# Performance work log

Hardware: AMD Instinct MI355X
Metric: run time of the kernel (lower is better)

Reference implementation:

```python
import jax, jax.numpy as jnp
import numpy as np

N_HEAD = 16
EPS = 1e-5
ROPE_BASE = 10000.0


def setup_inputs() -> dict:
    key = jax.random.key(0)
    ks = jax.random.split(key, 6)
    B, T, C = 2, 2048, 1024
    s = 0.02  # typical GPT init scale
    return {
        "x": jax.random.normal(ks[0], (B, T, C), dtype=jnp.float32),
        "wq": jax.random.normal(ks[1], (C, C), dtype=jnp.float32) * s,
        "wk": jax.random.normal(ks[2], (C, C), dtype=jnp.float32) * s,
        "wv": jax.random.normal(ks[3], (C, C), dtype=jnp.float32) * s,
        "wproj": jax.random.normal(ks[4], (C, C), dtype=jnp.float32) * s,
        "g_rms": jnp.ones((C // N_HEAD,), dtype=jnp.float32),
    }


def reference(x, wq, wk, wv, wproj, g_rms):
    B, T, C = x.shape
    H = N_HEAD
    hd = C // H

    # QKV projections (torch Linear: y = x @ W.T), split into heads -> [B,T,H,hd]
    q = (x @ wq.T).reshape(B, T, H, hd)
    k = (x @ wk.T).reshape(B, T, H, hd)
    v = (x @ wv.T).reshape(B, T, H, hd)

    # RMSNorm over head_dim on q and k
    def rms(t):
        var = jnp.mean(t * t, axis=-1, keepdims=True) + EPS
        return g_rms * (t * jax.lax.rsqrt(var))

    q, k = rms(q), rms(k)

    # Rotary embeddings: cos/sin cached in bf16 in the original -> bf16 round-trip
    inv_freq = 1.0 / (ROPE_BASE ** (jnp.arange(0, hd, 2, dtype=jnp.float32) / hd))
    freqs = jnp.outer(jnp.arange(T, dtype=jnp.float32), inv_freq)  # [T, hd/2]
    cos = jnp.cos(freqs).astype(jnp.bfloat16).astype(jnp.float32)[None, :, None, :]
    sin = jnp.sin(freqs).astype(jnp.bfloat16).astype(jnp.float32)[None, :, None, :]

    def rope(u):
        d = hd // 2
        u1, u2 = u[..., :d], u[..., d:]
        return jnp.concatenate([u1 * cos + u2 * sin, -u1 * sin + u2 * cos], axis=-1)

    q, k = rope(q), rope(k)

    # Attention: float ones attn_mask => constant +1.0 bias (softmax-invariant);
    # NOT causal (is_causal defaults False); dropout_p = 0.
    qh = q.transpose(0, 2, 1, 3)  # [B,H,T,hd]
    kh = k.transpose(0, 2, 1, 3)
    vh = v.transpose(0, 2, 1, 3)
    scale = 1.0 / jnp.sqrt(jnp.float32(hd))
    scores = jnp.einsum('bhtd,bhsd->bhts', qh, kh) * scale + 1.0  # [B,H,T,T]
    attn = jax.nn.softmax(scores, axis=-1)
    y = jnp.einsum('bhts,bhsd->bhtd', attn, vh)

    y = y.transpose(0, 2, 1, 3).reshape(B, T, C)
    return y @ wproj.T
```

## Files before the change

### kernel.cpp

```cpp
#include <hip/hip_runtime.h>
#include <hip/hip_bf16.h>
#include <stdint.h>

typedef __attribute__((ext_vector_type(8))) short short8;
typedef __attribute__((ext_vector_type(4))) float f32x4;
typedef __attribute__((ext_vector_type(16))) float f32x16;
typedef __attribute__((ext_vector_type(4))) unsigned short ushort4v;
typedef __attribute__((ext_vector_type(4))) unsigned int uint4v;

#define TT 2048
#define HH 16
#define CCdim 1024
#define BT 4096
#define LOG2E 1.44269504088896f

__device__ inline unsigned short f2bf(float f) {
  unsigned u = __float_as_uint(f);
  u += 0x7FFF + ((u >> 16) & 1);
  return (unsigned short)(u >> 16);
}
__device__ inline float bf2f(unsigned short s) {
  return __uint_as_float(((unsigned)s) << 16);
}
__device__ inline unsigned pack2(float a, float b) {
  return (unsigned)f2bf(a) | ((unsigned)f2bf(b) << 16);
}
__device__ inline unsigned cvtpk(float lo, float hi) {
  unsigned r;
  asm("v_cvt_pk_bf16_f32 %0, %1, %2" : "=v"(r) : "v"(lo), "v"(hi));
  return r;
}
__device__ inline void plswap(unsigned &a, unsigned &b) {
  asm("v_permlane32_swap_b32 %0, %1" : "+v"(a), "+v"(b));
}

__device__ inline void gload16(const unsigned short* g, unsigned short* l) {
  __builtin_amdgcn_global_load_lds((const __attribute__((address_space(1))) void*)g,
                                   (__attribute__((address_space(3))) void*)l, 16, 0, 0);
}

#define VMB(N) do { asm volatile("s_waitcnt vmcnt(" #N ")" ::: "memory"); \
                    __builtin_amdgcn_s_barrier(); \
                    __builtin_amdgcn_sched_barrier(0); } while (0)

__global__ __launch_bounds__(256) void prep(const float* __restrict__ x, const float* __restrict__ wq,
                     const float* __restrict__ wk, const float* __restrict__ wv,
                     const float* __restrict__ wp, unsigned short* __restrict__ xb,
                     unsigned short* __restrict__ wqkv, unsigned short* __restrict__ wpb,
                     float2* __restrict__ tab) {
  long idx = ((long)blockIdx.x * 256 + threadIdx.x) * 4;
  const long NX = (long)BT * CCdim;
  const long NW = (long)CCdim * CCdim;
  auto cvt4 = [](const float* src, unsigned short* dst, long off) {
    float4 v = *(const float4*)(src + off);
    ushort4v o = { f2bf(v.x), f2bf(v.y), f2bf(v.z), f2bf(v.w) };
    *(ushort4v*)(dst + off) = o;
  };
  if (idx < NX) { cvt4(x, xb, idx); return; }
  idx -= NX;
  if (idx < NW) { cvt4(wq, wqkv, idx); return; }
  idx -= NW;
  if (idx < NW) { cvt4(wk, wqkv + NW, idx); return; }
  idx -= NW;
  if (idx < NW) { cvt4(wv, wqkv + 2 * NW, idx); return; }
  idx -= NW;
  if (idx < NW) { cvt4(wp, wpb, idx); return; }
  idx -= NW;
  if (idx < (long)TT * 32) {
#pragma unroll
    for (int j = 0; j < 4; ++j) {
      long e = idx + j;
      int t = (int)(e >> 5), i = (int)(e & 31);
      float invf = powf(10000.0f, -(float)i / 32.0f);
      float a = (float)t * invf;
      tab[e] = make_float2(bf2f(f2bf(cosf(a))), bf2f(f2bf(sinf(a))));
    }
  }
}

__global__ __launch_bounds__(256) void gemm_qkv(const unsigned short* __restrict__ A,
                                                const unsigned short* __restrict__ W,
                                                const float* __restrict__ g,
                                                const float2* __restrict__ tab,
                                                unsigned short* __restrict__ Qh,
                                                unsigned short* __restrict__ Kp,
                                                unsigned short* __restrict__ Vp) {
  __shared__ __align__(16) char smem[49152];
  unsigned short* const S0 = (unsigned short*)smem;
  unsigned short* const S1 = S0 + 8192;
  unsigned short* const S2 = S0 + 16384;
  typedef unsigned short (*Earr)[64][68];
  Earr E = (Earr)smem;
  const int K = 1024;
  const int tid = threadIdx.x;
  const int lane = tid & 63;
  const int wid = tid >> 6;
  const int wr = wid >> 1, wc = wid & 1;
  const int m0 = blockIdx.y * 128;
  const int n0 = blockIdx.x * 128;

  f32x4 acc[4][4] = {};

  const int srow0 = tid >> 2;
  const int cgrp = tid & 3;
  const int cd = (cgrp ^ ((srow0 >> 1) & 3)) * 8;
  const unsigned short* Arow0 = A + (long)(m0 + srow0) * K + cd;
  const unsigned short* Arow1 = A + (long)(m0 + srow0 + 64) * K + cd;
  const unsigned short* Wrow0 = W + (long)(n0 + srow0) * K + cd;
  const unsigned short* Wrow1 = W + (long)(n0 + srow0 + 64) * K + cd;

  auto stage = [&](unsigned short* Ab, int kt) {
    const int kof = kt * 32;
    gload16(Arow0 + kof, Ab + wid * 512);
    gload16(Arow1 + kof, Ab + 2048 + wid * 512);
    gload16(Wrow0 + kof, Ab + 4096 + wid * 512);
    gload16(Wrow1 + kof, Ab + 6144 + wid * 512);
  };
  auto compute = [&](const unsigned short* Ab) {
    const unsigned short* Wb = Ab + 4096;
    short8 af[4], bf[4];
#pragma unroll
    for (int mi = 0; mi < 4; ++mi) {
      int r = wr * 64 + mi * 16 + (lane & 15);
      af[mi] = *(const short8*)&Ab[r * 32 + (((lane >> 4) ^ ((r >> 1) & 3)) * 8)];
    }
#pragma unroll
    for (int nj = 0; nj < 4; ++nj) {
      int r = wc * 64 + nj * 16 + (lane & 15);
      bf[nj] = *(const short8*)&Wb[r * 32 + (((lane >> 4) ^ ((r >> 1) & 3)) * 8)];
    }
#pragma unroll
    for (int mi = 0; mi < 4; ++mi)
#pragma unroll
      for (int nj = 0; nj < 4; ++nj)
        acc[mi][nj] = __builtin_amdgcn_mfma_f32_16x16x32_bf16(af[mi], bf[nj], acc[mi][nj], 0, 0, 0);
  };

  stage(S0, 0);
  stage(S1, 1);
  for (int tb = 0; tb < 30; tb += 3) {
    VMB(4); stage(S2, tb + 2); compute(S0);
    VMB(4); stage(S0, tb + 3); compute(S1);
    VMB(4); stage(S1, tb + 4); compute(S2);
  }
  VMB(4); compute(S0);
  VMB(0); compute(S1);
  __syncthreads();

  const int type = blockIdx.x >> 3;
  const int c0 = n0 + wc * 64;
  const int b = m0 >> 11;
  const int t0w = (m0 & 2047) + wr * 64;
  const int bh = b * 16 + ((c0 >> 6) & 15);
  const int cl = lane & 15;
  const int hi4 = lane >> 4;

  if (type < 2) {
    float gv0 = g[cl], gv1 = g[cl + 16], gv2 = g[cl + 32], gv3 = g[cl + 48];
    const float qs = (type == 0) ? 0.125f * LOG2E : 1.0f;
#pragma unroll
    for (int mi = 0; mi < 4; ++mi)
#pragma unroll
      for (int j = 0; j < 4; ++j) {
        float x0 = acc[mi][0][j], x1 = acc[mi][1][j], x2 = acc[mi][2][j], x3 = acc[mi][3][j];
        float ss = x0 * x0 + x1 * x1 + x2 * x2 + x3 * x3;
        ss += __shfl_xor(ss, 1); ss += __shfl_xor(ss, 2);
        ss += __shfl_xor(ss, 4); ss += __shfl_xor(ss, 8);
        float ri = rsqrtf(ss * (1.0f / 64.0f) + 1e-5f);
        float xn0 = x0 * ri * gv0, xn1 = x1 * ri * gv1;
        float xn2 = x2 * ri * gv2, xn3 = x3 * ri * gv3;
        int t = t0w + mi * 16 + 4 * hi4 + j;
        float2 cs0 = tab[t * 32 + cl];
        float2 cs1 = tab[t * 32 + cl + 16];
        int lr = mi * 16 + 4 * hi4 + j;
        E[wid][lr][cl]      = f2bf((xn0 * cs0.x + xn2 * cs0.y) * qs);
        E[wid][lr][cl + 16] = f2bf((xn1 * cs1.x + xn3 * cs1.y) * qs);
        E[wid][lr][cl + 32] = f2bf((xn2 * cs0.x - xn0 * cs0.y) * qs);
        E[wid][lr][cl + 48] = f2bf((xn3 * cs1.x - xn1 * cs1.y) * qs);
      }
  } else {
#pragma unroll
    for (int mi = 0; mi < 4; ++mi)
#pragma unroll
      for (int j = 0; j < 4; ++j) {
        int lr = mi * 16 + 4 * hi4 + j;
        E[wid][lr][cl]      = f2bf(acc[mi][0][j]);
        E[wid][lr][cl + 16] = f2bf(acc[mi][1][j]);
        E[wid][lr][cl + 32] = f2bf(acc[mi][2][j]);
        E[wid][lr][cl + 48] = f2bf(acc[mi][3][j]);
      }
  }
  __syncthreads();

  if (type == 0) {
    for (int row = 0; row < 64; ++row) {
      int t = t0w + row;
      Qh[((long)bh * TT + t) * 64 + lane] = E[wid][row][lane];
    }
  } else if (type == 1) {
    for (int row = 0; row < 64; ++row) {
      int t = t0w + row;
      Kp[(((long)bh * 64 + (t >> 5)) * 4 + (lane >> 4)) * 512
         + ((t & 31) + 32 * ((lane >> 3) & 1)) * 8 + (lane & 7)] = E[wid][row][lane];
    }
  } else {
    unsigned short* base = Vp + ((long)bh * 64 + (t0w >> 5)) * 2048;
#pragma unroll
    for (int it = 0; it < 8; ++it) {
      int id = it * 64 + lane;
      int cc = it & 1, sd = (it >> 1) & 1, ttloc = (it >> 2) & 1;
      int d = sd * 32 + (lane & 31);
      int tl = ttloc * 32 + cc * 16 + (lane >> 5) * 8;
      short8 o;
#pragma unroll
      for (int jj = 0; jj < 8; ++jj) o[jj] = (short)E[wid][tl + jj][d];
      *(short8*)(base + (long)id * 8) = o;
    }
  }
}

__global__ __launch_bounds__(256) void gemm_bt(const unsigned short* __restrict__ A,
                                               const unsigned short* __restrict__ W,
                                               float* __restrict__ C, int ldc) {
  __shared__ __align__(16) unsigned short Sbuf[3][8192];
  unsigned short* const S0 = &Sbuf[0][0];
  unsigned short* const S1 = &Sbuf[1][0];
  unsigned short* const S2 = &Sbuf[2][0];
  const int K = 1024;
  const int tid = threadIdx.x;
  const int lane = tid & 63;
  const int wid = tid >> 6;
  const int wr = wid >> 1, wc = wid & 1;
  const int m0 = blockIdx.y * 128;
  const int n0 = blockIdx.x * 128;

  f32x4 acc[4][4] = {};

  const int srow0 = tid >> 2;
  const int cgrp = tid & 3;
  const int cd = (cgrp ^ ((srow0 >> 1) & 3)) * 8;
  const unsigned short* Arow0 = A + (long)(m0 + srow0) * K + cd;
  const unsigned short* Arow1 = A + (long)(m0 + srow0 + 64) * K + cd;
  const unsigned short* Wrow0 = W + (long)(n0 + srow0) * K + cd;
  const unsigned short* Wrow1 = W + (long)(n0 + srow0 + 64) * K + cd;

  auto stage = [&](unsigned short* Ab, int kt) {
    const int kof = kt * 32;
    gload16(Arow0 + kof, Ab + wid * 512);
    gload16(Arow1 + kof, Ab + 2048 + wid * 512);
    gload16(Wrow0 + kof, Ab + 4096 + wid * 512);
    gload16(Wrow1 + kof, Ab + 6144 + wid * 512);
  };
  auto compute = [&](const unsigned short* Ab) {
    const unsigned short* Wb = Ab + 4096;
    short8 af[4], bf[4];
#pragma unroll
    for (int mi = 0; mi < 4; ++mi) {
      int r = wr * 64 + mi * 16 + (lane & 15);
      af[mi] = *(const short8*)&Ab[r * 32 + (((lane >> 4) ^ ((r >> 1) & 3)) * 8)];
    }
#pragma unroll
    for (int nj = 0; nj < 4; ++nj) {
      int r = wc * 64 + nj * 16 + (lane & 15);
      bf[nj] = *(const short8*)&Wb[r * 32 + (((lane >> 4) ^ ((r >> 1) & 3)) * 8)];
    }
#pragma unroll
    for (int mi = 0; mi < 4; ++mi)
#pragma unroll
      for (int nj = 0; nj < 4; ++nj)
        acc[mi][nj] = __builtin_amdgcn_mfma_f32_16x16x32_bf16(af[mi], bf[nj], acc[mi][nj], 0, 0, 0);
  };

  stage(S0, 0);
  stage(S1, 1);
  for (int tb = 0; tb < 30; tb += 3) {
    VMB(4); stage(S2, tb + 2); compute(S0);
    VMB(4); stage(S0, tb + 3); compute(S1);
    VMB(4); stage(S1, tb + 4); compute(S2);
  }
  VMB(4); compute(S0);
  VMB(0); compute(S1);

#pragma unroll
  for (int mi = 0; mi < 4; ++mi)
#pragma unroll
    for (int nj = 0; nj < 4; ++nj)
#pragma unroll
      for (int j = 0; j < 4; ++j) {
        int rr = m0 + wr * 64 + mi * 16 + 4 * (lane >> 4) + j;
        int ncol = n0 + wc * 64 + nj * 16 + (lane & 15);
        C[(long)rr * ldc + ncol] = acc[mi][nj][j];
      }
}

__global__ __launch_bounds__(256, 2) void attn(const unsigned short* __restrict__ Qh,
                                               const unsigned short* __restrict__ Kp,
                                               const unsigned short* __restrict__ Vp,
                                               float* __restrict__ Opart,
                                               float* __restrict__ L) {
  const int lane = threadIdx.x & 63;
  const int wid = threadIdx.x >> 6;
  int bid = blockIdx.x;
  bid = (bid & 7) * 64 + (bid >> 3);
  const int w = bid * 4 + wid;
  const int qt = w & 31;
  const int half = (w >> 5) & 1;
  const int bh = w >> 6;
  const long bhT = (long)bh * TT;
  const int q0 = qt * 64;
  const int l31 = lane & 31;
  const int hk = (lane >> 5) * 8;

  short8 qf[4], qg[4];
  {
    const unsigned short* qp = Qh + (bhT + q0 + l31) * 64 + hk;
#pragma unroll
    for (int c = 0; c < 4; ++c) {
      qf[c] = *(const short8*)(qp + c * 16);
      qg[c] = *(const short8*)(qp + 2048 + c * 16);
    }
  }

  const unsigned short* kp = Kp + ((long)(bh * 64 + half * 32)) * 2048 + lane * 8;
  const unsigned short* vp = Vp + ((long)(bh * 64 + half * 32)) * 2048 + lane * 8;

  f32x16 oacc0 = {}, oacc1 = {}, oacc2 = {}, oacc3 = {};
  float ell = 0.f, ell2 = 0.f;

  short8 kA[4], vA0[2], vA1[2], kB[4], vB0[2], vB1[2];
#pragma unroll
  for (int c = 0; c < 4; ++c) kA[c] = *(const short8*)(kp + c * 512);
#pragma unroll
  for (int c = 0; c < 2; ++c) {
    vA0[c] = *(const short8*)(vp + c * 512);
    vA1[c] = *(const short8*)(vp + 1024 + c * 512);
  }

  auto body = [&](short8 (&kc)[4], short8 (&v0c)[2], short8 (&v1c)[2],
                  short8 (&knx)[4], short8 (&v0n)[2], short8 (&v1n)[2], int tn) {
    const unsigned short* kpn = kp + tn * 2048;
    const unsigned short* vpn = vp + tn * 2048;
#pragma unroll
    for (int c = 0; c < 4; ++c) knx[c] = *(const short8*)(kpn + c * 512);
#pragma unroll
    for (int c = 0; c < 2; ++c) {
      v0n[c] = *(const short8*)(vpn + c * 512);
      v1n[c] = *(const short8*)(vpn + 1024 + c * 512);
    }

    __builtin_amdgcn_s_setprio(1);
    f32x16 s = {}, s2 = {};
#pragma unroll
    for (int c = 0; c < 4; ++c) {
      s  = __builtin_amdgcn_mfma_f32_32x32x16_bf16(kc[c], qf[c], s, 0, 0, 0);
      s2 = __builtin_amdgcn_mfma_f32_32x32x16_bf16(kc[c], qg[c], s2, 0, 0, 0);
    }
    __builtin_amdgcn_s_setprio(0);

#pragma unroll
    for (int r = 0; r < 16; ++r) s[r] = __builtin_amdgcn_exp2f(s[r]);
#pragma unroll
    for (int r = 0; r < 16; ++r) s2[r] = __builtin_amdgcn_exp2f(s2[r]);
    {
      float t0 = s[0] + s[1], t1 = s[2] + s[3], t2s = s[4] + s[5], t3 = s[6] + s[7];
      float t4 = s[8] + s[9], t5 = s[10] + s[11], t6 = s[12] + s[13], t7 = s[14] + s[15];
      t0 += t1; t2s += t3; t4 += t5; t6 += t7;
      ell += (t0 + t2s) + (t4 + t6);
    }
    {
      float t0 = s2[0] + s2[1], t1 = s2[2] + s2[3], t2s = s2[4] + s2[5], t3 = s2[6] + s2[7];
      float t4 = s2[8] + s2[9], t5 = s2[10] + s2[11], t6 = s2[12] + s2[13], t7 = s2[14] + s2[15];
      t0 += t1; t2s += t3; t4 += t5; t6 += t7;
      ell2 += (t0 + t2s) + (t4 + t6);
    }

    unsigned a0 = cvtpk(s[0], s[1]),   a1 = cvtpk(s[2], s[3]);
    unsigned a2 = cvtpk(s[4], s[5]),   a3 = cvtpk(s[6], s[7]);
    unsigned a4 = cvtpk(s[8], s[9]),   a5 = cvtpk(s[10], s[11]);
    unsigned a6 = cvtpk(s[12], s[13]), a7 = cvtpk(s[14], s[15]);
    plswap(a0, a2); plswap(a1, a3); plswap(a4, a6); plswap(a5, a7);
    uint4v f0 = { a0, a1, a2, a3 };
    uint4v f1 = { a4, a5, a6, a7 };
    short8 pf0 = __builtin_bit_cast(short8, f0);
    short8 pf1 = __builtin_bit_cast(short8, f1);

    unsigned b0 = cvtpk(s2[0], s2[1]),   b1 = cvtpk(s2[2], s2[3]);
    unsigned b2 = cvtpk(s2[4], s2[5]),   b3 = cvtpk(s2[6], s2[7]);
    unsigned b4 = cvtpk(s2[8], s2[9]),   b5 = cvtpk(s2[10], s2[11]);
    unsigned b6 = cvtpk(s2[12], s2[13]), b7 = cvtpk(s2[14], s2[15]);
    plswap(b0, b2); plswap(b1, b3); plswap(b4, b6); plswap(b5, b7);
    uint4v g0 = { b0, b1, b2, b3 };
    uint4v g1 = { b4, b5, b6, b7 };
    short8 pg0 = __builtin_bit_cast(short8, g0);
    short8 pg1 = __builtin_bit_cast(short8, g1);

    __builtin_amdgcn_s_setprio(1);
    oacc0 = __builtin_amdgcn_mfma_f32_32x32x16_bf16(v0c[0], pf0, oacc0, 0, 0, 0);
    oacc0 = __builtin_amdgcn_mfma_f32_32x32x16_bf16(v0c[1], pf1, oacc0, 0, 0, 0);
    oacc1 = __builtin_amdgcn_mfma_f32_32x32x16_bf16(v1c[0], pf0, oacc1, 0, 0, 0);
    oacc1 = __builtin_amdgcn_mfma_f32_32x32x16_bf16(v1c[1], pf1, oacc1, 0, 0, 0);
    oacc2 = __builtin_amdgcn_mfma_f32_32x32x16_bf16(v0c[0], pg0, oacc2, 0, 0, 0);
    oacc2 = __builtin_amdgcn_mfma_f32_32x32x16_bf16(v0c[1], pg1, oacc2, 0, 0, 0);
    oacc3 = __builtin_amdgcn_mfma_f32_32x32x16_bf16(v1c[0], pg0, oacc3, 0, 0, 0);
    oacc3 = __builtin_amdgcn_mfma_f32_32x32x16_bf16(v1c[1], pg1, oacc3, 0, 0, 0);
    __builtin_amdgcn_s_setprio(0);
  };

  for (int t = 0; t < 32; t += 2) {
    int t1 = t + 1;
    int t2 = (t < 30) ? (t + 2) : 31;
    body(kA, vA0, vA1, kB, vB0, vB1, t1);
    body(kB, vB0, vB1, kA, vA0, vA1, t2);
  }

  float ellf  = ell + __shfl_xor(ell, 32);
  float ellf2 = ell2 + __shfl_xor(ell2, 32);
  const long prow = (long)(half * 32 + bh) * TT + q0 + l31;
  float* orow  = Opart + prow * 64;
  float* orow2 = orow + 32 * 64;
  const int dhalf = 4 * (lane >> 5);
#pragma unroll
  for (int i = 0; i < 8; ++i) {
    int d = (2 * i & 3) + 8 * (i >> 1) + dhalf;
    *(float2*)&orow[d]       = make_float2(oacc0[2 * i], oacc0[2 * i + 1]);
    *(float2*)&orow[32 + d]  = make_float2(oacc1[2 * i], oacc1[2 * i + 1]);
    *(float2*)&orow2[d]      = make_float2(oacc2[2 * i], oacc2[2 * i + 1]);
    *(float2*)&orow2[32 + d] = make_float2(oacc3[2 * i], oacc3[2 * i + 1]);
  }
  if (lane < 32) { L[prow] = ellf; L[prow + 32] = ellf2; }
}

__global__ __launch_bounds__(256) void combine(const float* __restrict__ Opart,
                                               const float* __restrict__ L,
                                               unsigned short* __restrict__ Y) {
  const long HALF = (long)32 * TT * 64;
  int idx = blockIdx.x * 256 + threadIdx.x;
  int row = idx >> 5;
  int d = (idx & 31) * 2;
  float2 o0 = *(const float2*)&Opart[(long)row * 64 + d];
  float2 o1 = *(const float2*)&Opart[HALF + (long)row * 64 + d];
  float rinv = 1.0f / (L[row] + L[65536 + row]);
  float ox = (o0.x + o1.x) * rinv;
  float oy = (o0.y + o1.y) * rinv;
  int bh = row >> 11, qrow = row & (TT - 1);
  int b = bh >> 4, h = bh & 15;
  *(unsigned*)&Y[((long)(b * TT + qrow)) * CCdim + h * 64 + d] = pack2(ox, oy);
}

extern "C" void kernel_launch(void* const* d_in, const int* in_sizes, int n_in,
                              void* d_out, int out_size, void* d_ws, size_t ws_size,
                              hipStream_t stream) {
  const float* x  = (const float*)d_in[0];
  const float* wq = (const float*)d_in[1];
  const float* wk = (const float*)d_in[2];
  const float* wv = (const float*)d_in[3];
  const float* wp = (const float*)d_in[4];
  const float* g  = (const float*)d_in[5];

  char* w = (char*)d_ws;
  unsigned short* xb   = (unsigned short*)w; w += (long)BT * CCdim * 2;
  unsigned short* wqkv = (unsigned short*)w; w += (long)3 * CCdim * CCdim * 2;
  unsigned short* wpb  = (unsigned short*)w; w += (long)CCdim * CCdim * 2;
  unsigned short* qh   = (unsigned short*)w; w += (long)BT * CCdim * 2;
  unsigned short* kp   = (unsigned short*)w; w += (long)BT * CCdim * 2;
  unsigned short* vp   = (unsigned short*)w; w += (long)BT * CCdim * 2;
  unsigned short* yb   = (unsigned short*)w; w += (long)BT * CCdim * 2;
  float2* tab          = (float2*)w;         w += (long)TT * 32 * 8;
  float* Opart         = (float*)w;          w += (long)64 * TT * 64 * 4;
  float* Lbuf          = (float*)w;          w += (long)64 * TT * 4;

  long total = ((long)BT * CCdim + 4L * CCdim * CCdim + (long)TT * 32) / 4;
  int pblocks = (int)((total + 255) / 256);
  prep<<<pblocks, 256, 0, stream>>>(x, wq, wk, wv, wp, xb, wqkv, wpb, tab);
  gemm_qkv<<<dim3(24, 32), 256, 0, stream>>>(xb, wqkv, g, tab, qh, kp, vp);
  attn<<<512, 256, 0, stream>>>(qh, kp, vp, Opart, Lbuf);
  combine<<<8192, 256, 0, stream>>>(Opart, Lbuf, yb);
  gemm_bt<<<dim3(8, 32), 256, 0, stream>>>(yb, wpb, (float*)d_out, 1024);
}
```

Before: 127.4 us.

## Fuse split-KV combine into attention via LDS and swizzle GEMM blocks per XCD

The attention kernel now puts both KV halves of a query tile in the same workgroup. One wave writes its partial output and row sums to LDS, and the partner wave merges them, normalizes, and writes bf16 Y directly. This removes the fp32 partial-output round trip through global memory and the separate combine launch. Both GEMMs also remap block indices so each XCD works on a contiguous group of tiles, which should improve L2 reuse. The cost is extra LDS use in attention (about 33KB) and a block-wide barrier, which may reduce occupancy.

```diff
diff --git a/kernel.cpp b/kernel.cpp
--- a/kernel.cpp
+++ b/kernel.cpp
@@ -96,8 +96,12 @@
   const int lane = tid & 63;
   const int wid = tid >> 6;
   const int wr = wid >> 1, wc = wid & 1;
-  const int m0 = blockIdx.y * 128;
-  const int n0 = blockIdx.x * 128;
+  const int bid0 = blockIdx.y * 24 + blockIdx.x;
+  const int xcd = bid0 & 7, ii = bid0 >> 3;
+  const int bx = (xcd & 1) * 12 + ii % 12;
+  const int by = (xcd >> 1) * 8 + ii / 12;
+  const int m0 = by * 128;
+  const int n0 = bx * 128;
 
   f32x4 acc[4][4] = {};
 
@@ -147,7 +151,7 @@
   VMB(0); compute(S1);
   __syncthreads();
 
-  const int type = blockIdx.x >> 3;
+  const int type = bx >> 3;
   const int c0 = n0 + wc * 64;
   const int b = m0 >> 11;
   const int t0w = (m0 & 2047) + wr * 64;
@@ -231,8 +235,10 @@
   const int lane = tid & 63;
   const int wid = tid >> 6;
   const int wr = wid >> 1, wc = wid & 1;
-  const int m0 = blockIdx.y * 128;
-  const int n0 = blockIdx.x * 128;
+  const int bid0 = blockIdx.y * 8 + blockIdx.x;
+  const int xcd = bid0 & 7, ii = bid0 >> 3;
+  const int m0 = (xcd * 4 + ii / 8) * 128;
+  const int n0 = (ii & 7) * 128;
 
   f32x4 acc[4][4] = {};
 
@@ -296,15 +302,16 @@
 __global__ __launch_bounds__(256, 2) void attn(const unsigned short* __restrict__ Qh,
                                                const unsigned short* __restrict__ Kp,
                                                const unsigned short* __restrict__ Vp,
-                                               float* __restrict__ Opart,
-                                               float* __restrict__ L) {
+                                               unsigned short* __restrict__ Y) {
+  __shared__ __align__(16) float Obuf[2][64][65];
+  __shared__ float Ebuf[2][64];
   const int lane = threadIdx.x & 63;
   const int wid = threadIdx.x >> 6;
   int bid = blockIdx.x;
   bid = (bid & 7) * 64 + (bid >> 3);
   const int w = bid * 4 + wid;
-  const int qt = w & 31;
-  const int half = (w >> 5) & 1;
+  const int half = w & 1;
+  const int qt = (w >> 1) & 31;
   const int bh = w >> 6;
   const long bhT = (long)bh * TT;
   const int q0 = qt * 64;
@@ -415,36 +422,44 @@
 
   float ellf  = ell + __shfl_xor(ell, 32);
   float ellf2 = ell2 + __shfl_xor(ell2, 32);
-  const long prow = (long)(half * 32 + bh) * TT + q0 + l31;
-  float* orow  = Opart + prow * 64;
-  float* orow2 = orow + 32 * 64;
+  const int pl = wid >> 1;
   const int dhalf = 4 * (lane >> 5);
-#pragma unroll
-  for (int i = 0; i < 8; ++i) {
-    int d = (2 * i & 3) + 8 * (i >> 1) + dhalf;
-    *(float2*)&orow[d]       = make_float2(oacc0[2 * i], oacc0[2 * i + 1]);
-    *(float2*)&orow[32 + d]  = make_float2(oacc1[2 * i], oacc1[2 * i + 1]);
-    *(float2*)&orow2[d]      = make_float2(oacc2[2 * i], oacc2[2 * i + 1]);
-    *(float2*)&orow2[32 + d] = make_float2(oacc3[2 * i], oacc3[2 * i + 1]);
-  }
-  if (lane < 32) { L[prow] = ellf; L[prow + 32] = ellf2; }
-}
-
-__global__ __launch_bounds__(256) void combine(const float* __restrict__ Opart,
-                                               const float* __restrict__ L,
-                                               unsigned short* __restrict__ Y) {
-  const long HALF = (long)32 * TT * 64;
-  int idx = blockIdx.x * 256 + threadIdx.x;
-  int row = idx >> 5;
-  int d = (idx & 31) * 2;
-  float2 o0 = *(const float2*)&Opart[(long)row * 64 + d];
-  float2 o1 = *(const float2*)&Opart[HALF + (long)row * 64 + d];
-  float rinv = 1.0f / (L[row] + L[65536 + row]);
-  float ox = (o0.x + o1.x) * rinv;
-  float oy = (o0.y + o1.y) * rinv;
-  int bh = row >> 11, qrow = row & (TT - 1);
-  int b = bh >> 4, h = bh & 15;
-  *(unsigned*)&Y[((long)(b * TT + qrow)) * CCdim + h * 64 + d] = pack2(ox, oy);
+
+  if (half) {
+#pragma unroll
+    for (int i = 0; i < 8; ++i) {
+      int d = (2 * i & 3) + 8 * (i >> 1) + dhalf;
+      *(float2*)&Obuf[pl][l31][d]           = make_float2(oacc0[2 * i], oacc0[2 * i + 1]);
+      *(float2*)&Obuf[pl][l31][32 + d]      = make_float2(oacc1[2 * i], oacc1[2 * i + 1]);
+      *(float2*)&Obuf[pl][l31 + 32][d]      = make_float2(oacc2[2 * i], oacc2[2 * i + 1]);
+      *(float2*)&Obuf[pl][l31 + 32][32 + d] = make_float2(oacc3[2 * i], oacc3[2 * i + 1]);
+    }
+    if (lane < 32) { Ebuf[pl][l31] = ellf; Ebuf[pl][l31 + 32] = ellf2; }
+  }
+  __syncthreads();
+  if (!half) {
+    const int b = bh >> 4, h = bh & 15;
+    float r1 = 1.0f / (ellf + Ebuf[pl][l31]);
+    float r2 = 1.0f / (ellf2 + Ebuf[pl][l31 + 32]);
+    long base1 = ((long)b * TT + q0 + l31) * CCdim + h * 64;
+    long base2 = base1 + (long)32 * CCdim;
+#pragma unroll
+    for (int i = 0; i < 8; ++i) {
+      int d = (2 * i & 3) + 8 * (i >> 1) + dhalf;
+      *(unsigned*)&Y[base1 + d] =
+        pack2((oacc0[2 * i] + Obuf[pl][l31][d]) * r1,
+              (oacc0[2 * i + 1] + Obuf[pl][l31][d + 1]) * r1);
+      *(unsigned*)&Y[base1 + 32 + d] =
+        pack2((oacc1[2 * i] + Obuf[pl][l31][32 + d]) * r1,
+              (oacc1[2 * i + 1] + Obuf[pl][l31][32 + d + 1]) * r1);
+      *(unsigned*)&Y[base2 + d] =
+        pack2((oacc2[2 * i] + Obuf[pl][l31 + 32][d]) * r2,
+              (oacc2[2 * i + 1] + Obuf[pl][l31 + 32][d + 1]) * r2);
+      *(unsigned*)&Y[base2 + 32 + d] =
+        pack2((oacc3[2 * i] + Obuf[pl][l31 + 32][32 + d]) * r2,
+              (oacc3[2 * i + 1] + Obuf[pl][l31 + 32][32 + d + 1]) * r2);
+    }
+  }
 }
 
 extern "C" void kernel_launch(void* const* d_in, const int* in_sizes, int n_in,
@@ -466,14 +481,11 @@
   unsigned short* vp   = (unsigned short*)w; w += (long)BT * CCdim * 2;
   unsigned short* yb   = (unsigned short*)w; w += (long)BT * CCdim * 2;
   float2* tab          = (float2*)w;         w += (long)TT * 32 * 8;
-  float* Opart         = (float*)w;          w += (long)64 * TT * 64 * 4;
-  float* Lbuf          = (float*)w;          w += (long)64 * TT * 4;
 
   long total = ((long)BT * CCdim + 4L * CCdim * CCdim + (long)TT * 32) / 4;
   int pblocks = (int)((total + 255) / 256);
   prep<<<pblocks, 256, 0, stream>>>(x, wq, wk, wv, wp, xb, wqkv, wpb, tab);
   gemm_qkv<<<dim3(24, 32), 256, 0, stream>>>(xb, wqkv, g, tab, qh, kp, vp);
-  attn<<<512, 256, 0, stream>>>(qh, kp, vp, Opart, Lbuf);
-  combine<<<8192, 256, 0, stream>>>(Opart, Lbuf, yb);
+  attn<<<512, 256, 0, stream>>>(qh, kp, vp, yb);
   gemm_bt<<<dim3(8, 32), 256, 0, stream>>>(yb, wpb, (float*)d_out, 1024);
 }
```

After: 111.6 us. -12.4%, faster.
